# Performance work log

Hardware: AMD Instinct MI355X
Metric: run time of the kernel (lower is better)

Reference implementation:

```python
import math
import jax, jax.numpy as jnp
import numpy as np

INPUT_DIM = 512
HIDDEN_DIM = 512
BATCH = 8
SEQ_LEN = 4096


def _xavier(key, shape):
    fan_out, fan_in = shape
    limit = math.sqrt(6.0 / (fan_in + fan_out))
    return jax.random.uniform(key, shape, jnp.float32, -limit, limit)


def setup_inputs() -> dict:
    key = jax.random.key(0)
    kx, kA, kB, kC, kD, kWg = jax.random.split(key, 6)
    return {
        "x": jax.random.normal(kx, (BATCH, SEQ_LEN, INPUT_DIM), jnp.float32),
        "A": jax.random.uniform(kA, (HIDDEN_DIM,), jnp.float32, 0.8, 0.95),
        "B": _xavier(kB, (HIDDEN_DIM, INPUT_DIM)),
        "C": _xavier(kC, (HIDDEN_DIM, HIDDEN_DIM)),
        "D": _xavier(kD, (HIDDEN_DIM, INPUT_DIM)),
        "Wg": _xavier(kWg, (HIDDEN_DIM, INPUT_DIM)),
        "bias_h": jnp.zeros((HIDDEN_DIM,), jnp.float32),
        "bias_y": jnp.zeros((HIDDEN_DIM,), jnp.float32),
    }


def reference(x, A, B, C, D, Wg, bias_h, bias_y):
    # x: (b, t, i). Eval mode: dropout is identity.
    hidden_dim = A.shape[0]
    # Precompute all input-dependent per-step terms as batched GEMMs.
    g = jnp.clip(jax.nn.sigmoid(jnp.einsum('bti,hi->bth', x, Wg)), 0.05, 0.95)
    xB = jnp.einsum('bti,hi->bth', x, B)
    # h_t = h_{t-1} + g_t*(A*h_{t-1} + xB_t + bias_h - h_{t-1})
    #     = (1 - g_t*(1 - A)) * h_{t-1} + g_t*(xB_t + bias_h)
    a_coef = 1.0 - g * (1.0 - A)          # (b, t, h)
    b_coef = g * (xB + bias_h)            # (b, t, h)

    def step(h, ab):
        a_t, b_t = ab
        h = a_t * h + b_t
        return h, h

    h0 = jnp.zeros((x.shape[0], hidden_dim), x.dtype)
    _, hs = jax.lax.scan(step, h0, (jnp.swapaxes(a_coef, 0, 1), jnp.swapaxes(b_coef, 0, 1)))
    hs = jnp.swapaxes(hs, 0, 1)           # (b, t, h)

    scale = 1.0 / math.sqrt(hidden_dim)
    y = (jnp.einsum('bth,oh->bto', hs, C) + jnp.einsum('bti,hi->bth', x, D) + bias_y) * scale
    return y
```

## Files before the change

### kernel.cpp

```cpp
#include <hip/hip_runtime.h>
#include <math.h>

#define MTOT 32768
#define KD 512
#define HD 512
#define NB 8
#define TS 4096
#define NCHUNK 64
#define TCHUNK 64

typedef __attribute__((ext_vector_type(8))) short bf16x8;
typedef __attribute__((ext_vector_type(4))) float f32x4;
typedef __attribute__((ext_vector_type(4))) unsigned short us4;

#define GLD16(gsrc, ldst) __builtin_amdgcn_global_load_lds( \
    (const __attribute__((address_space(1))) void*)(gsrc),   \
    (__attribute__((address_space(3))) void*)(ldst), 16, 0, 0)

__device__ __forceinline__ unsigned short f2bf(float f) {
    unsigned u = __float_as_uint(f);
    return (unsigned short)((u + 0x7FFFu + ((u >> 16) & 1u)) >> 16);
}
__device__ __forceinline__ float bf2f(unsigned short u) {
    return __uint_as_float(((unsigned)u) << 16);
}

__global__ __launch_bounds__(256) void cast_all(
    const float* __restrict__ x, const float* __restrict__ B,
    const float* __restrict__ G, const float* __restrict__ C,
    const float* __restrict__ D,
    unsigned short* __restrict__ x16, unsigned short* __restrict__ w16)
{
    const int blk = blockIdx.x;
    const float* src;
    unsigned short* dst;
    int i;
    if (blk < (MTOT * KD / 1024)) {
        src = x; dst = x16;
        i = blk * 1024 + threadIdx.x * 4;
    } else {
        const int r = blk - (MTOT * KD / 1024);
        const int mat = r >> 8;
        src = (mat == 0) ? B : (mat == 1) ? G : (mat == 2) ? C : D;
        dst = w16 + (size_t)mat * (HD * KD);
        i = (r & 255) * 1024 + threadIdx.x * 4;
    }
    float4 v = *(const float4*)(src + i);
    us4 o; o.x = f2bf(v.x); o.y = f2bf(v.y); o.z = f2bf(v.z); o.w = f2bf(v.w);
    *(us4*)(dst + i) = o;
}

__global__ __launch_bounds__(256, 3) void in_gemm_mfma(
    const short* __restrict__ xb, const short* __restrict__ wmat,
    const float* __restrict__ Avec, const float* __restrict__ bias_h,
    unsigned* __restrict__ ab16, float2* __restrict__ chPS)
{
    __shared__ __align__(16) short Xs[128 * 64];
    __shared__ __align__(16) short Ws[2][64 * 64];
    const int tid = threadIdx.x;
    const int w = tid >> 6, l = tid & 63;
    const int m0 = blockIdx.x * 128;
    const int n0 = blockIdx.y * 64;
    const int wm = (w & 1) * 64;
    const int wn = (w >> 1) * 32;

    int xsrc[4], xdst[4];
    #pragma unroll
    for (int j = 0; j < 4; ++j) {
        const int s = (w * 4 + j) * 64 + l;
        const int r = s >> 3, g = (s & 7) ^ (r & 7);
        xsrc[j] = (m0 + r) * KD + g * 8;
        xdst[j] = (w * 4 + j) * 64 * 8;
    }
    int wsrc[2], wdst[2];
    #pragma unroll
    for (int j = 0; j < 2; ++j) {
        const int s = (w * 2 + j) * 64 + l;
        const int r = s >> 3, g = (s & 7) ^ (r & 7);
        wsrc[j] = (n0 + r) * KD + g * 8;
        wdst[j] = (w * 2 + j) * 64 * 8;
    }

    f32x4 acc[2][4][2];
    #pragma unroll
    for (int a = 0; a < 2; ++a)
        #pragma unroll
        for (int i = 0; i < 4; ++i)
            #pragma unroll
            for (int j = 0; j < 2; ++j) acc[a][i][j] = (f32x4)0.0f;

    for (int kk = 0; kk < KD; kk += 64) {
        __syncthreads();
        #pragma unroll
        for (int j = 0; j < 4; ++j) GLD16(xb + xsrc[j] + kk, Xs + xdst[j]);
        #pragma unroll
        for (int mat = 0; mat < 2; ++mat)
            #pragma unroll
            for (int j = 0; j < 2; ++j)
                GLD16(wmat + (size_t)mat * (HD * KD) + wsrc[j] + kk, &Ws[mat][wdst[j]]);
        __syncthreads();
        #pragma unroll
        for (int kc = 0; kc < 2; ++kc) {
            const int g = kc * 4 + (l >> 4);
            bf16x8 af[4];
            #pragma unroll
            for (int mt = 0; mt < 4; ++mt) {
                const int r = wm + mt * 16 + (l & 15);
                af[mt] = *(const bf16x8*)(Xs + r * 64 + ((g ^ (r & 7)) * 8));
            }
            #pragma unroll
            for (int mat = 0; mat < 2; ++mat) {
                #pragma unroll
                for (int nt = 0; nt < 2; ++nt) {
                    const int r = wn + nt * 16 + (l & 15);
                    bf16x8 bfv = *(const bf16x8*)(&Ws[mat][r * 64 + ((g ^ (r & 7)) * 8)]);
                    #pragma unroll
                    for (int mt = 0; mt < 4; ++mt)
                        acc[mat][mt][nt] = __builtin_amdgcn_mfma_f32_16x16x32_bf16(
                            af[mt], bfv, acc[mat][mt][nt], 0, 0, 0);
                }
            }
        }
    }

    const int q  = l >> 4;
    const int cl = l & 15;
    const int bidx   = m0 >> 12;
    const int c_in_b = ((m0 & (TS - 1)) >> 6) + (w & 1);
    #pragma unroll
    for (int nt = 0; nt < 2; ++nt) {
        const int n = n0 + wn + nt * 16 + cl;
        const float An1 = 1.0f - Avec[n];
        const float bh  = bias_h[n];
        float Pc = 1.0f, Sc = 0.0f;
        #pragma unroll
        for (int mt = 0; mt < 4; ++mt) {
            float Pl = 1.0f, Sl = 0.0f;
            #pragma unroll
            for (int r = 0; r < 4; ++r) {
                const float vB = acc[0][mt][nt][r];
                const float vG = acc[1][mt][nt][r];
                float g = __builtin_amdgcn_rcpf(1.0f + __expf(-vG));
                g = fminf(fmaxf(g, 0.05f), 0.95f);
                const unsigned short su = f2bf(g * An1);
                const unsigned short bu = f2bf(g * (vB + bh));
                const float a  = 1.0f - bf2f(su);
                const float bb = bf2f(bu);
                const int m = m0 + wm + mt * 16 + q * 4 + r;
                ab16[(size_t)m * HD + n] = (unsigned)su | ((unsigned)bu << 16);
                Sl = fmaf(a, Sl, bb);
                Pl *= a;
            }
            float Pm = 1.0f, Sm = 0.0f;
            #pragma unroll
            for (int k = 0; k < 4; ++k) {
                const float Pk = __shfl(Pl, cl + 16 * k, 64);
                const float Sk = __shfl(Sl, cl + 16 * k, 64);
                Sm = fmaf(Pk, Sm, Sk);
                Pm *= Pk;
            }
            Sc = fmaf(Pm, Sc, Sm);
            Pc *= Pm;
        }
        if (q == 0) {
            chPS[(size_t)c_in_b * (NB * HD) + bidx * HD + n] = make_float2(Pc, Sc);
        }
    }
}

__global__ __launch_bounds__(256) void scan_pass3(
    const unsigned* __restrict__ ab, const float2* __restrict__ chPS,
    unsigned short* __restrict__ hs_out)
{
    const int g = blockIdx.x * blockDim.x + threadIdx.x;
    const int h = g & (HD - 1);
    const int rest = g >> 9;
    const int b = rest & (NB - 1);
    const int c = rest >> 3;
    const float2* p = chPS + (size_t)b * HD + h;
    float hv = 0.0f;
    for (int j = 0; j < c; ++j) {
        const float2 ps = p[(size_t)j * (NB * HD)];
        hv = fmaf(ps.x, hv, ps.y);
    }
    size_t idx = ((size_t)(b * TS + c * TCHUNK)) * HD + h;
    #pragma unroll 4
    for (int t = 0; t < TCHUNK; ++t) {
        const unsigned v = ab[idx];
        const float a  = 1.0f - bf2f((unsigned short)(v & 0xFFFFu));
        const float bb = bf2f((unsigned short)(v >> 16));
        hv = fmaf(a, hv, bb);
        hs_out[idx] = f2bf(hv);
        idx += HD;
    }
}

__global__ __launch_bounds__(256, 2) void out_gemm_dual(
    const short* __restrict__ hs, const short* __restrict__ xb,
    const short* __restrict__ Cb, const short* __restrict__ Db,
    const float* __restrict__ bias_y, float* __restrict__ y)
{
    __shared__ __align__(16) short Hs[128 * 64];
    __shared__ __align__(16) short Xs2[128 * 64];
    __shared__ __align__(16) short Cs[128 * 64];
    __shared__ __align__(16) short Ds[128 * 64];
    const int tid = threadIdx.x;
    const int w = tid >> 6, l = tid & 63;
    const int m0 = blockIdx.x * 128;
    const int n0 = blockIdx.y * 128;
    const int wm = (w & 1) * 64;
    const int wn = (w >> 1) * 64;

    int src_m[4], src_n[4], dst_s[4];
    #pragma unroll
    for (int j = 0; j < 4; ++j) {
        const int s = (w * 4 + j) * 64 + l;
        const int r = s >> 3, g = (s & 7) ^ (r & 7);
        src_m[j] = (m0 + r) * HD + g * 8;
        src_n[j] = (n0 + r) * HD + g * 8;
        dst_s[j] = (w * 4 + j) * 64 * 8;
    }

    f32x4 acc[4][4];
    #pragma unroll
    for (int i = 0; i < 4; ++i)
        #pragma unroll
        for (int j = 0; j < 4; ++j) acc[i][j] = (f32x4)0.0f;

    for (int kk = 0; kk < HD; kk += 64) {
        __syncthreads();
        #pragma unroll
        for (int j = 0; j < 4; ++j) {
            GLD16(hs + src_m[j] + kk, Hs  + dst_s[j]);
            GLD16(xb + src_m[j] + kk, Xs2 + dst_s[j]);
            GLD16(Cb + src_n[j] + kk, Cs  + dst_s[j]);
            GLD16(Db + src_n[j] + kk, Ds  + dst_s[j]);
        }
        __syncthreads();
        #pragma unroll
        for (int kc = 0; kc < 2; ++kc) {
            const int g = kc * 4 + (l >> 4);
            {
                bf16x8 af[4], bfv[4];
                #pragma unroll
                for (int t = 0; t < 4; ++t) {
                    const int ra = wm + t * 16 + (l & 15);
                    af[t] = *(const bf16x8*)(Hs + ra * 64 + ((g ^ (ra & 7)) * 8));
                    const int rb = wn + t * 16 + (l & 15);
                    bfv[t] = *(const bf16x8*)(Cs + rb * 64 + ((g ^ (rb & 7)) * 8));
                }
                #pragma unroll
                for (int mt = 0; mt < 4; ++mt)
                    #pragma unroll
                    for (int nt = 0; nt < 4; ++nt)
                        acc[mt][nt] = __builtin_amdgcn_mfma_f32_16x16x32_bf16(
                            af[mt], bfv[nt], acc[mt][nt], 0, 0, 0);
            }
            {
                bf16x8 af[4], bfv[4];
                #pragma unroll
                for (int t = 0; t < 4; ++t) {
                    const int ra = wm + t * 16 + (l & 15);
                    af[t] = *(const bf16x8*)(Xs2 + ra * 64 + ((g ^ (ra & 7)) * 8));
                    const int rb = wn + t * 16 + (l & 15);
                    bfv[t] = *(const bf16x8*)(Ds + rb * 64 + ((g ^ (rb & 7)) * 8));
                }
                #pragma unroll
                for (int mt = 0; mt < 4; ++mt)
                    #pragma unroll
                    for (int nt = 0; nt < 4; ++nt)
                        acc[mt][nt] = __builtin_amdgcn_mfma_f32_16x16x32_bf16(
                            af[mt], bfv[nt], acc[mt][nt], 0, 0, 0);
            }
        }
    }

    const float scale = 0.04419417382415922f;
    #pragma unroll
    for (int nt = 0; nt < 4; ++nt) {
        const int n = n0 + wn + nt * 16 + (l & 15);
        const float by = bias_y[n];
        #pragma unroll
        for (int mt = 0; mt < 4; ++mt) {
            #pragma unroll
            for (int r = 0; r < 4; ++r) {
                const int m = m0 + wm + mt * 16 + (l >> 4) * 4 + r;
                y[(size_t)m * HD + n] = (acc[mt][nt][r] + by) * scale;
            }
        }
    }
}

extern "C" void kernel_launch(void* const* d_in, const int* in_sizes, int n_in,
                              void* d_out, int out_size, void* d_ws, size_t ws_size,
                              hipStream_t stream) {
    const float* x      = (const float*)d_in[0];
    const float* Avec   = (const float*)d_in[1];
    const float* Bw     = (const float*)d_in[2];
    const float* Cw     = (const float*)d_in[3];
    const float* Dw     = (const float*)d_in[4];
    const float* Wg     = (const float*)d_in[5];
    const float* bias_h = (const float*)d_in[6];
    const float* bias_y = (const float*)d_in[7];
    float* y = (float*)d_out;

    unsigned* ab16        = (unsigned*)d_ws;
    unsigned short* x16   = (unsigned short*)(ab16 + (size_t)MTOT * HD);
    unsigned short* hs16  = x16 + (size_t)MTOT * HD;
    unsigned short* w16   = hs16 + (size_t)MTOT * HD;
    float2* chPS = (float2*)(w16 + (size_t)4 * HD * KD);

    cast_all<<<MTOT * KD / 1024 + 4 * (HD * KD / 1024), 256, 0, stream>>>(
        x, Bw, Wg, Cw, Dw, x16, w16);

    in_gemm_mfma<<<dim3(MTOT / 128, HD / 64), 256, 0, stream>>>(
        (const short*)x16, (const short*)w16, Avec, bias_h, ab16, chPS);

    scan_pass3<<<(NB * HD * NCHUNK) / 256, 256, 0, stream>>>(ab16, chPS, hs16);

    out_gemm_dual<<<dim3(MTOT / 128, HD / 128), 256, 0, stream>>>(
        (const short*)hs16, (const short*)x16,
        (const short*)(w16 + (size_t)2 * HD * KD),
        (const short*)(w16 + (size_t)3 * HD * KD), bias_y, y);
}
```

Before: 249.1 us.

## Double-buffer activation tiles and read weights directly from global in both GEMMs

Both input and output GEMMs now keep only the activation tile in LDS, double-buffered with async global-to-LDS loads and explicit waitcnt/barrier so the next K-slice loads while the current one computes. Weight fragments are read straight from global memory (expected to hit L2/L1) instead of being staged in LDS. The grid is transposed so neighbouring blocks share the same M rows and sweep N. This cuts LDS use and raises occupancy, at the cost of uncoalesced per-lane global weight loads sitting on the MFMA critical path.

```diff
diff --git a/kernel.cpp b/kernel.cpp
--- a/kernel.cpp
+++ b/kernel.cpp
@@ -50,17 +50,16 @@
     *(us4*)(dst + i) = o;
 }
 
-__global__ __launch_bounds__(256, 3) void in_gemm_mfma(
+__global__ __launch_bounds__(256, 4) void in_gemm_mfma(
     const short* __restrict__ xb, const short* __restrict__ wmat,
     const float* __restrict__ Avec, const float* __restrict__ bias_h,
     unsigned* __restrict__ ab16, float2* __restrict__ chPS)
 {
-    __shared__ __align__(16) short Xs[128 * 64];
-    __shared__ __align__(16) short Ws[2][64 * 64];
+    __shared__ __align__(16) short Xs[2][128 * 64];
     const int tid = threadIdx.x;
     const int w = tid >> 6, l = tid & 63;
-    const int m0 = blockIdx.x * 128;
-    const int n0 = blockIdx.y * 64;
+    const int n0 = blockIdx.x * 64;
+    const int m0 = blockIdx.y * 128;
     const int wm = (w & 1) * 64;
     const int wn = (w >> 1) * 32;
 
@@ -72,14 +71,6 @@
         xsrc[j] = (m0 + r) * KD + g * 8;
         xdst[j] = (w * 4 + j) * 64 * 8;
     }
-    int wsrc[2], wdst[2];
-    #pragma unroll
-    for (int j = 0; j < 2; ++j) {
-        const int s = (w * 2 + j) * 64 + l;
-        const int r = s >> 3, g = (s & 7) ^ (r & 7);
-        wsrc[j] = (n0 + r) * KD + g * 8;
-        wdst[j] = (w * 2 + j) * 64 * 8;
-    }
 
     f32x4 acc[2][4][2];
     #pragma unroll
@@ -89,16 +80,26 @@
             #pragma unroll
             for (int j = 0; j < 2; ++j) acc[a][i][j] = (f32x4)0.0f;
 
-    for (int kk = 0; kk < KD; kk += 64) {
-        __syncthreads();
-        #pragma unroll
-        for (int j = 0; j < 4; ++j) GLD16(xb + xsrc[j] + kk, Xs + xdst[j]);
-        #pragma unroll
-        for (int mat = 0; mat < 2; ++mat)
-            #pragma unroll
-            for (int j = 0; j < 2; ++j)
-                GLD16(wmat + (size_t)mat * (HD * KD) + wsrc[j] + kk, &Ws[mat][wdst[j]]);
-        __syncthreads();
+    const int nrow0 = n0 + wn + (l & 15);
+
+    #pragma unroll
+    for (int j = 0; j < 4; ++j) GLD16(xb + xsrc[j], &Xs[0][xdst[j]]);
+
+    #pragma unroll
+    for (int it = 0; it < 8; ++it) {
+        const int cur = it & 1;
+        const int kk = it * 64;
+        asm volatile("s_waitcnt lgkmcnt(0)" ::: "memory");
+        __builtin_amdgcn_s_barrier();
+        if (it < 7) {
+            #pragma unroll
+            for (int j = 0; j < 4; ++j)
+                GLD16(xb + xsrc[j] + kk + 64, &Xs[cur ^ 1][xdst[j]]);
+            asm volatile("s_waitcnt vmcnt(4)" ::: "memory");
+        } else {
+            asm volatile("s_waitcnt vmcnt(0)" ::: "memory");
+        }
+        __builtin_amdgcn_s_barrier();
         #pragma unroll
         for (int kc = 0; kc < 2; ++kc) {
             const int g = kc * 4 + (l >> 4);
@@ -106,14 +107,15 @@
             #pragma unroll
             for (int mt = 0; mt < 4; ++mt) {
                 const int r = wm + mt * 16 + (l & 15);
-                af[mt] = *(const bf16x8*)(Xs + r * 64 + ((g ^ (r & 7)) * 8));
+                af[mt] = *(const bf16x8*)(&Xs[cur][r * 64 + ((g ^ (r & 7)) * 8)]);
             }
             #pragma unroll
             for (int mat = 0; mat < 2; ++mat) {
                 #pragma unroll
                 for (int nt = 0; nt < 2; ++nt) {
-                    const int r = wn + nt * 16 + (l & 15);
-                    bf16x8 bfv = *(const bf16x8*)(&Ws[mat][r * 64 + ((g ^ (r & 7)) * 8)]);
+                    bf16x8 bfv = *(const bf16x8*)(
+                        wmat + (size_t)mat * (HD * KD)
+                             + (size_t)(nrow0 + nt * 16) * KD + kk + g * 8);
                     #pragma unroll
                     for (int mt = 0; mt < 4; ++mt)
                         acc[mat][mt][nt] = __builtin_amdgcn_mfma_f32_16x16x32_bf16(
@@ -200,24 +202,21 @@
     const short* __restrict__ Cb, const short* __restrict__ Db,
     const float* __restrict__ bias_y, float* __restrict__ y)
 {
-    __shared__ __align__(16) short Hs[128 * 64];
-    __shared__ __align__(16) short Xs2[128 * 64];
-    __shared__ __align__(16) short Cs[128 * 64];
-    __shared__ __align__(16) short Ds[128 * 64];
+    __shared__ __align__(16) short Hs[2][128 * 64];
+    __shared__ __align__(16) short Xs2[2][128 * 64];
     const int tid = threadIdx.x;
     const int w = tid >> 6, l = tid & 63;
-    const int m0 = blockIdx.x * 128;
-    const int n0 = blockIdx.y * 128;
+    const int n0 = blockIdx.x * 128;
+    const int m0 = blockIdx.y * 128;
     const int wm = (w & 1) * 64;
     const int wn = (w >> 1) * 64;
 
-    int src_m[4], src_n[4], dst_s[4];
+    int src_m[4], dst_s[4];
     #pragma unroll
     for (int j = 0; j < 4; ++j) {
         const int s = (w * 4 + j) * 64 + l;
         const int r = s >> 3, g = (s & 7) ^ (r & 7);
         src_m[j] = (m0 + r) * HD + g * 8;
-        src_n[j] = (n0 + r) * HD + g * 8;
         dst_s[j] = (w * 4 + j) * 64 * 8;
     }
 
@@ -227,16 +226,31 @@
         #pragma unroll
         for (int j = 0; j < 4; ++j) acc[i][j] = (f32x4)0.0f;
 
-    for (int kk = 0; kk < HD; kk += 64) {
-        __syncthreads();
-        #pragma unroll
-        for (int j = 0; j < 4; ++j) {
-            GLD16(hs + src_m[j] + kk, Hs  + dst_s[j]);
-            GLD16(xb + src_m[j] + kk, Xs2 + dst_s[j]);
-            GLD16(Cb + src_n[j] + kk, Cs  + dst_s[j]);
-            GLD16(Db + src_n[j] + kk, Ds  + dst_s[j]);
-        }
-        __syncthreads();
+    const int nrow0 = n0 + wn + (l & 15);
+
+    #pragma unroll
+    for (int j = 0; j < 4; ++j) {
+        GLD16(hs + src_m[j], &Hs[0][dst_s[j]]);
+        GLD16(xb + src_m[j], &Xs2[0][dst_s[j]]);
+    }
+
+    #pragma unroll
+    for (int it = 0; it < 8; ++it) {
+        const int cur = it & 1;
+        const int kk = it * 64;
+        asm volatile("s_waitcnt lgkmcnt(0)" ::: "memory");
+        __builtin_amdgcn_s_barrier();
+        if (it < 7) {
+            #pragma unroll
+            for (int j = 0; j < 4; ++j) {
+                GLD16(hs + src_m[j] + kk + 64, &Hs[cur ^ 1][dst_s[j]]);
+                GLD16(xb + src_m[j] + kk + 64, &Xs2[cur ^ 1][dst_s[j]]);
+            }
+            asm volatile("s_waitcnt vmcnt(8)" ::: "memory");
+        } else {
+            asm volatile("s_waitcnt vmcnt(0)" ::: "memory");
+        }
+        __builtin_amdgcn_s_barrier();
         #pragma unroll
         for (int kc = 0; kc < 2; ++kc) {
             const int g = kc * 4 + (l >> 4);
@@ -245,9 +259,9 @@
                 #pragma unroll
                 for (int t = 0; t < 4; ++t) {
                     const int ra = wm + t * 16 + (l & 15);
-                    af[t] = *(const bf16x8*)(Hs + ra * 64 + ((g ^ (ra & 7)) * 8));
-                    const int rb = wn + t * 16 + (l & 15);
-                    bfv[t] = *(const bf16x8*)(Cs + rb * 64 + ((g ^ (rb & 7)) * 8));
+                    af[t] = *(const bf16x8*)(&Hs[cur][ra * 64 + ((g ^ (ra & 7)) * 8)]);
+                    bfv[t] = *(const bf16x8*)(
+                        Cb + (size_t)(nrow0 + t * 16) * HD + kk + g * 8);
                 }
                 #pragma unroll
                 for (int mt = 0; mt < 4; ++mt)
@@ -261,9 +275,9 @@
                 #pragma unroll
                 for (int t = 0; t < 4; ++t) {
                     const int ra = wm + t * 16 + (l & 15);
-                    af[t] = *(const bf16x8*)(Xs2 + ra * 64 + ((g ^ (ra & 7)) * 8));
-                    const int rb = wn + t * 16 + (l & 15);
-                    bfv[t] = *(const bf16x8*)(Ds + rb * 64 + ((g ^ (rb & 7)) * 8));
+                    af[t] = *(const bf16x8*)(&Xs2[cur][ra * 64 + ((g ^ (ra & 7)) * 8)]);
+                    bfv[t] = *(const bf16x8*)(
+                        Db + (size_t)(nrow0 + t * 16) * HD + kk + g * 8);
                 }
                 #pragma unroll
                 for (int mt = 0; mt < 4; ++mt)
@@ -313,12 +327,12 @@
     cast_all<<<MTOT * KD / 1024 + 4 * (HD * KD / 1024), 256, 0, stream>>>(
         x, Bw, Wg, Cw, Dw, x16, w16);
 
-    in_gemm_mfma<<<dim3(MTOT / 128, HD / 64), 256, 0, stream>>>(
+    in_gemm_mfma<<<dim3(HD / 64, MTOT / 128), 256, 0, stream>>>(
         (const short*)x16, (const short*)w16, Avec, bias_h, ab16, chPS);
 
     scan_pass3<<<(NB * HD * NCHUNK) / 256, 256, 0, stream>>>(ab16, chPS, hs16);
 
-    out_gemm_dual<<<dim3(MTOT / 128, HD / 128), 256, 0, stream>>>(
+    out_gemm_dual<<<dim3(HD / 128, MTOT / 128), 256, 0, stream>>>(
         (const short*)hs16, (const short*)x16,
         (const short*)(w16 + (size_t)2 * HD * KD),
         (const short*)(w16 + (size_t)3 * HD * KD), bias_y, y);
```

New measurement: 329.2 us. 32.1% more time.

## Double-buffer LDS tiles in both MFMA GEMMs to overlap loads with compute

Applied to the files above, without the earlier changes.

Both the input GEMM and the output dual-GEMM now use two LDS buffers. The next K-tile is prefetched with global_load_lds while the current tile runs through MFMA, and each iteration ends with a single vmcnt wait plus barrier instead of two syncthreads. The output GEMM also restructures its dual GEMM as one 16-step K loop over concatenated [hs|x] and [C|D] operands, which keeps LDS the same size while allowing double buffering. The input GEMM's LDS doubles and its occupancy hint drops from 3 to 2 blocks, trading latency hiding for fewer resident waves. s_setprio is raised around the MFMA section.

```diff
diff --git a/kernel.cpp b/kernel.cpp
--- a/kernel.cpp
+++ b/kernel.cpp
@@ -50,13 +50,13 @@
     *(us4*)(dst + i) = o;
 }
 
-__global__ __launch_bounds__(256, 3) void in_gemm_mfma(
+__global__ __launch_bounds__(256, 2) void in_gemm_mfma(
     const short* __restrict__ xb, const short* __restrict__ wmat,
     const float* __restrict__ Avec, const float* __restrict__ bias_h,
     unsigned* __restrict__ ab16, float2* __restrict__ chPS)
 {
-    __shared__ __align__(16) short Xs[128 * 64];
-    __shared__ __align__(16) short Ws[2][64 * 64];
+    __shared__ __align__(16) short Xs[2][128 * 64];
+    __shared__ __align__(16) short Ws[2][2][64 * 64];
     const int tid = threadIdx.x;
     const int w = tid >> 6, l = tid & 63;
     const int m0 = blockIdx.x * 128;
@@ -89,16 +89,32 @@
             #pragma unroll
             for (int j = 0; j < 2; ++j) acc[a][i][j] = (f32x4)0.0f;
 
-    for (int kk = 0; kk < KD; kk += 64) {
-        __syncthreads();
-        #pragma unroll
-        for (int j = 0; j < 4; ++j) GLD16(xb + xsrc[j] + kk, Xs + xdst[j]);
-        #pragma unroll
-        for (int mat = 0; mat < 2; ++mat)
-            #pragma unroll
-            for (int j = 0; j < 2; ++j)
-                GLD16(wmat + (size_t)mat * (HD * KD) + wsrc[j] + kk, &Ws[mat][wdst[j]]);
-        __syncthreads();
+    #pragma unroll
+    for (int j = 0; j < 4; ++j) GLD16(xb + xsrc[j], &Xs[0][xdst[j]]);
+    #pragma unroll
+    for (int mat = 0; mat < 2; ++mat)
+        #pragma unroll
+        for (int j = 0; j < 2; ++j)
+            GLD16(wmat + (size_t)mat * (HD * KD) + wsrc[j], &Ws[0][mat][wdst[j]]);
+    asm volatile("s_waitcnt vmcnt(0)" ::: "memory");
+    __builtin_amdgcn_s_barrier();
+
+    #pragma unroll
+    for (int it = 0; it < 8; ++it) {
+        const int cur = it & 1;
+        const int kk = it * 64;
+        if (it < 7) {
+            #pragma unroll
+            for (int j = 0; j < 4; ++j)
+                GLD16(xb + xsrc[j] + kk + 64, &Xs[cur ^ 1][xdst[j]]);
+            #pragma unroll
+            for (int mat = 0; mat < 2; ++mat)
+                #pragma unroll
+                for (int j = 0; j < 2; ++j)
+                    GLD16(wmat + (size_t)mat * (HD * KD) + wsrc[j] + kk + 64,
+                          &Ws[cur ^ 1][mat][wdst[j]]);
+        }
+        __builtin_amdgcn_s_setprio(1);
         #pragma unroll
         for (int kc = 0; kc < 2; ++kc) {
             const int g = kc * 4 + (l >> 4);
@@ -106,14 +122,14 @@
             #pragma unroll
             for (int mt = 0; mt < 4; ++mt) {
                 const int r = wm + mt * 16 + (l & 15);
-                af[mt] = *(const bf16x8*)(Xs + r * 64 + ((g ^ (r & 7)) * 8));
+                af[mt] = *(const bf16x8*)(&Xs[cur][r * 64 + ((g ^ (r & 7)) * 8)]);
             }
             #pragma unroll
             for (int mat = 0; mat < 2; ++mat) {
                 #pragma unroll
                 for (int nt = 0; nt < 2; ++nt) {
                     const int r = wn + nt * 16 + (l & 15);
-                    bf16x8 bfv = *(const bf16x8*)(&Ws[mat][r * 64 + ((g ^ (r & 7)) * 8)]);
+                    bf16x8 bfv = *(const bf16x8*)(&Ws[cur][mat][r * 64 + ((g ^ (r & 7)) * 8)]);
                     #pragma unroll
                     for (int mt = 0; mt < 4; ++mt)
                         acc[mat][mt][nt] = __builtin_amdgcn_mfma_f32_16x16x32_bf16(
@@ -121,6 +137,9 @@
                 }
             }
         }
+        __builtin_amdgcn_s_setprio(0);
+        asm volatile("s_waitcnt vmcnt(0)" ::: "memory");
+        __builtin_amdgcn_s_barrier();
     }
 
     const int q  = l >> 4;
@@ -200,10 +219,8 @@
     const short* __restrict__ Cb, const short* __restrict__ Db,
     const float* __restrict__ bias_y, float* __restrict__ y)
 {
-    __shared__ __align__(16) short Hs[128 * 64];
-    __shared__ __align__(16) short Xs2[128 * 64];
-    __shared__ __align__(16) short Cs[128 * 64];
-    __shared__ __align__(16) short Ds[128 * 64];
+    __shared__ __align__(16) short As[2][128 * 64];
+    __shared__ __align__(16) short Ws[2][128 * 64];
     const int tid = threadIdx.x;
     const int w = tid >> 6, l = tid & 63;
     const int m0 = blockIdx.x * 128;
@@ -211,69 +228,64 @@
     const int wm = (w & 1) * 64;
     const int wn = (w >> 1) * 64;
 
-    int src_m[4], src_n[4], dst_s[4];
+    int aoff[4], woff[4], dst_s[4];
     #pragma unroll
     for (int j = 0; j < 4; ++j) {
         const int s = (w * 4 + j) * 64 + l;
         const int r = s >> 3, g = (s & 7) ^ (r & 7);
-        src_m[j] = (m0 + r) * HD + g * 8;
-        src_n[j] = (n0 + r) * HD + g * 8;
+        aoff[j] = (m0 + r) * HD + g * 8;
+        woff[j] = (n0 + r) * HD + g * 8;
         dst_s[j] = (w * 4 + j) * 64 * 8;
     }
 
+#define STAGE_OUT(TI, BUF) do {                                         \
+    const short* abase_ = (((TI) < 8) ? hs : xb) + ((TI) & 7) * 64;     \
+    const short* wbase_ = (((TI) < 8) ? Cb : Db) + ((TI) & 7) * 64;     \
+    _Pragma("unroll")                                                   \
+    for (int j_ = 0; j_ < 4; ++j_) {                                    \
+        GLD16(abase_ + aoff[j_], &As[BUF][dst_s[j_]]);                  \
+        GLD16(wbase_ + woff[j_], &Ws[BUF][dst_s[j_]]);                  \
+    }                                                                   \
+} while (0)
+
     f32x4 acc[4][4];
     #pragma unroll
     for (int i = 0; i < 4; ++i)
         #pragma unroll
         for (int j = 0; j < 4; ++j) acc[i][j] = (f32x4)0.0f;
 
-    for (int kk = 0; kk < HD; kk += 64) {
-        __syncthreads();
-        #pragma unroll
-        for (int j = 0; j < 4; ++j) {
-            GLD16(hs + src_m[j] + kk, Hs  + dst_s[j]);
-            GLD16(xb + src_m[j] + kk, Xs2 + dst_s[j]);
-            GLD16(Cb + src_n[j] + kk, Cs  + dst_s[j]);
-            GLD16(Db + src_n[j] + kk, Ds  + dst_s[j]);
-        }
-        __syncthreads();
+    STAGE_OUT(0, 0);
+    asm volatile("s_waitcnt vmcnt(0)" ::: "memory");
+    __builtin_amdgcn_s_barrier();
+
+    #pragma unroll
+    for (int ti = 0; ti < 16; ++ti) {
+        const int cur = ti & 1;
+        if (ti < 15) STAGE_OUT(ti + 1, cur ^ 1);
+        __builtin_amdgcn_s_setprio(1);
         #pragma unroll
         for (int kc = 0; kc < 2; ++kc) {
             const int g = kc * 4 + (l >> 4);
-            {
-                bf16x8 af[4], bfv[4];
+            bf16x8 af[4], bfv[4];
+            #pragma unroll
+            for (int t = 0; t < 4; ++t) {
+                const int ra = wm + t * 16 + (l & 15);
+                af[t] = *(const bf16x8*)(&As[cur][ra * 64 + ((g ^ (ra & 7)) * 8)]);
+                const int rb = wn + t * 16 + (l & 15);
+                bfv[t] = *(const bf16x8*)(&Ws[cur][rb * 64 + ((g ^ (rb & 7)) * 8)]);
+            }
+            #pragma unroll
+            for (int mt = 0; mt < 4; ++mt)
                 #pragma unroll
-                for (int t = 0; t < 4; ++t) {
-                    const int ra = wm + t * 16 + (l & 15);
-                    af[t] = *(const bf16x8*)(Hs + ra * 64 + ((g ^ (ra & 7)) * 8));
-                    const int rb = wn + t * 16 + (l & 15);
-                    bfv[t] = *(const bf16x8*)(Cs + rb * 64 + ((g ^ (rb & 7)) * 8));
-                }
-                #pragma unroll
-                for (int mt = 0; mt < 4; ++mt)
-                    #pragma unroll
-                    for (int nt = 0; nt < 4; ++nt)
-                        acc[mt][nt] = __builtin_amdgcn_mfma_f32_16x16x32_bf16(
-                            af[mt], bfv[nt], acc[mt][nt], 0, 0, 0);
-            }
-            {
-                bf16x8 af[4], bfv[4];
-                #pragma unroll
-                for (int t = 0; t < 4; ++t) {
-                    const int ra = wm + t * 16 + (l & 15);
-                    af[t] = *(const bf16x8*)(Xs2 + ra * 64 + ((g ^ (ra & 7)) * 8));
-                    const int rb = wn + t * 16 + (l & 15);
-                    bfv[t] = *(const bf16x8*)(Ds + rb * 64 + ((g ^ (rb & 7)) * 8));
-                }
-                #pragma unroll
-                for (int mt = 0; mt < 4; ++mt)
-                    #pragma unroll
-                    for (int nt = 0; nt < 4; ++nt)
-                        acc[mt][nt] = __builtin_amdgcn_mfma_f32_16x16x32_bf16(
-                            af[mt], bfv[nt], acc[mt][nt], 0, 0, 0);
-            }
-        }
-    }
+                for (int nt = 0; nt < 4; ++nt)
+                    acc[mt][nt] = __builtin_amdgcn_mfma_f32_16x16x32_bf16(
+                        af[mt], bfv[nt], acc[mt][nt], 0, 0, 0);
+        }
+        __builtin_amdgcn_s_setprio(0);
+        asm volatile("s_waitcnt vmcnt(0)" ::: "memory");
+        __builtin_amdgcn_s_barrier();
+    }
+#undef STAGE_OUT
 
     const float scale = 0.04419417382415922f;
     #pragma unroll
```

Result: slower. 257.7 us (+3.5%).
